# Performance work log

Measured on AMD Instinct MI355X. Metric: run time of the kernel, lower is better.

## Reference

```python
import jax, jax.numpy as jnp
import numpy as np

N = 20000      # nodes
E = 320000     # edges (every node has >=1 incoming edge)
IN = 512       # input feature dim
HID = 128      # per-head hidden dim
H = 8          # heads
C = 64         # classes (final layer hidden dim)
SLOPE = 0.01   # torch F.leaky_relu default negative_slope


def _gat_head(x, src, dst, W, b, al, alb, ar, arb):
    # x: [N, D_in]; W: [D_in, D_h]; al/ar: [D_h]; alb/arb: scalar
    ft = x @ W + b                       # [N, D_h]
    a1 = ft @ al + alb                   # [N] dst-side logit
    a2 = ft @ ar + arb                   # [N] src-side logit
    s = jax.nn.leaky_relu(a1[dst] + a2[src], SLOPE)   # [E]
    smax = jax.ops.segment_max(s, dst, num_segments=N)
    e = jnp.exp(s - smax[dst])
    denom = jax.ops.segment_sum(e, dst, num_segments=N)
    w = e / denom[dst]                   # segment softmax over incoming edges
    accum = jax.ops.segment_sum(w[:, None] * ft[src], dst, num_segments=N)
    return jax.nn.elu(accum)             # GATFinalize (no residual)


def setup_inputs() -> dict:
    key = jax.random.key(0)
    ks = jax.random.split(key, 16)

    def lin(k, i, o):
        return (jax.random.normal(k, (i, o), jnp.float32) / np.sqrt(i))

    features = jax.random.normal(ks[0], (N, IN), jnp.float32)
    src = jax.random.randint(ks[1], (E,), 0, N, jnp.int32)
    dst = jnp.concatenate([
        jnp.arange(N, dtype=jnp.int32),
        jax.random.randint(ks[2], (E - N,), 0, N, jnp.int32),
    ])

    # layer 0: H heads, in_dim -> HID
    W0 = jax.random.normal(ks[3], (H, IN, HID), jnp.float32) / np.sqrt(IN)
    b0 = jnp.zeros((H, HID), jnp.float32)
    al0 = jax.random.normal(ks[4], (H, HID), jnp.float32) / np.sqrt(HID)
    alb0 = jnp.zeros((H,), jnp.float32)
    ar0 = jax.random.normal(ks[5], (H, HID), jnp.float32) / np.sqrt(HID)
    arb0 = jnp.zeros((H,), jnp.float32)

    # layer 1: H heads, H*HID -> HID
    W1 = jax.random.normal(ks[6], (H, H * HID, HID), jnp.float32) / np.sqrt(H * HID)
    b1 = jnp.zeros((H, HID), jnp.float32)
    al1 = jax.random.normal(ks[7], (H, HID), jnp.float32) / np.sqrt(HID)
    alb1 = jnp.zeros((H,), jnp.float32)
    ar1 = jax.random.normal(ks[8], (H, HID), jnp.float32) / np.sqrt(HID)
    arb1 = jnp.zeros((H,), jnp.float32)

    # final: single head, H*HID -> C
    Wf = lin(ks[9], H * HID, C)
    bf = jnp.zeros((C,), jnp.float32)
    alf = jax.random.normal(ks[10], (C,), jnp.float32) / np.sqrt(C)
    albf = jnp.zeros((), jnp.float32)
    arf = jax.random.normal(ks[11], (C,), jnp.float32) / np.sqrt(C)
    arbf = jnp.zeros((), jnp.float32)

    return dict(features=features, src=src, dst=dst,
                W0=W0, b0=b0, al0=al0, alb0=alb0, ar0=ar0, arb0=arb0,
                W1=W1, b1=b1, al1=al1, alb1=alb1, ar1=ar1, arb1=arb1,
                Wf=Wf, bf=bf, alf=alf, albf=albf, arf=arf, arbf=arbf)


def reference(features, src, dst,
              W0, b0, al0, alb0, ar0, arb0,
              W1, b1, al1, alb1, ar1, arb1,
              Wf, bf, alf, albf, arf, arbf):
    x = features
    # layer 0: concat heads -> [N, H*HID]
    x = jnp.concatenate([
        _gat_head(x, src, dst, W0[h], b0[h], al0[h], alb0[h], ar0[h], arb0[h])
        for h in range(H)], axis=1)
    # layer 1
    x = jnp.concatenate([
        _gat_head(x, src, dst, W1[h], b1[h], al1[h], alb1[h], ar1[h], arb1[h])
        for h in range(H)], axis=1)
    # final single-head output layer -> [N, C]
    return _gat_head(x, src, dst, Wf, bf, alf, albf, arf, arbf)
```

## Files before the change

kernel.cpp:

```cpp
#include <hip/hip_runtime.h>
#include <math.h>

#define N_NODES 20000
#define N_EDGES 320000
#define D_IN    512
#define D_HID   128
#define N_HEADS 8
#define N_CLS   64

typedef __bf16 bf16x8 __attribute__((ext_vector_type(8)));
typedef float  f32x4  __attribute__((ext_vector_type(4)));

__device__ __forceinline__ float leaky(float x) { return fmaxf(x, 0.01f * x); }

__device__ __forceinline__ unsigned short f2bf(float f) {
    unsigned u = __float_as_uint(f);
    return (unsigned short)((u + 0x7FFFu + ((u >> 16) & 1u)) >> 16);
}
__device__ __forceinline__ float bflo(unsigned v) { return __uint_as_float(v << 16); }
__device__ __forceinline__ float bfhi(unsigned v) { return __uint_as_float(v & 0xffff0000u); }

__device__ __forceinline__ void gl_lds16(const void* g, void* l) {
    __builtin_amdgcn_global_load_lds((const __attribute__((address_space(1))) void*)g,
                                     (__attribute__((address_space(3))) void*)l, 16, 0, 0);
}

__global__ void k_zero(int* __restrict__ p, int n) {
    int i = blockIdx.x * blockDim.x + threadIdx.x;
    if (i < n) p[i] = 0;
}

__global__ void k_count(const int* __restrict__ dst, int* __restrict__ counts, int e) {
    int i = blockIdx.x * blockDim.x + threadIdx.x;
    if (i < e) atomicAdd(&counts[dst[i]], 1);
}

__global__ void k_scan(const int* __restrict__ counts, int* __restrict__ indptr,
                       int* __restrict__ cursor, int n) {
    __shared__ int sdata[1024];
    __shared__ int srun;
    int t = threadIdx.x;
    if (t == 0) srun = 0;
    __syncthreads();
    for (int base = 0; base < n; base += 1024) {
        int idx = base + t;
        int v = (idx < n) ? counts[idx] : 0;
        sdata[t] = v;
        __syncthreads();
        for (int off = 1; off < 1024; off <<= 1) {
            int x = (t >= off) ? sdata[t - off] : 0;
            __syncthreads();
            sdata[t] += x;
            __syncthreads();
        }
        int incl = sdata[t];
        int run = srun;
        if (idx < n) {
            indptr[idx] = run + incl - v;
            cursor[idx] = run + incl - v;
        }
        __syncthreads();
        if (t == 1023) srun = run + incl;
        __syncthreads();
    }
    if (t == 0) indptr[n] = srun;
}

__global__ void k_scatter(const int* __restrict__ src, const int* __restrict__ dst,
                          int* __restrict__ cursor, int* __restrict__ csr_src, int e) {
    int i = blockIdx.x * blockDim.x + threadIdx.x;
    if (i < e) {
        int pos = atomicAdd(&cursor[dst[i]], 1);
        csr_src[pos] = src[i];
    }
}

__global__ void k_cvtA(const float* __restrict__ in, unsigned short* __restrict__ out, int n4) {
    int i = blockIdx.x * blockDim.x + threadIdx.x;
    if (i < n4) {
        float4 v = ((const float4*)in)[i];
        unsigned long long pk =
            (unsigned long long)f2bf(v.x) | ((unsigned long long)f2bf(v.y) << 16) |
            ((unsigned long long)f2bf(v.z) << 32) | ((unsigned long long)f2bf(v.w) << 48);
        *(unsigned long long*)(out + (size_t)i * 4) = pk;
    }
}

__global__ void k_cvtW(const float* __restrict__ W, unsigned short* __restrict__ Wt,
                       int K, int Nf) {
    __shared__ float t[64][65];
    int k0 = blockIdx.x * 64, n0 = blockIdx.y * 64, h = blockIdx.z;
    const float* Wh = W + (size_t)h * K * Nf;
    unsigned short* Wth = Wt + (size_t)h * K * Nf;
    int tx = threadIdx.x & 63, ty = threadIdx.x >> 6;
#pragma unroll
    for (int i = 0; i < 16; ++i) {
        int k = ty + i * 4;
        t[k][tx] = Wh[(size_t)(k0 + k) * Nf + n0 + tx];
    }
    __syncthreads();
#pragma unroll
    for (int i = 0; i < 16; ++i) {
        int n = ty + i * 4;
        Wth[(size_t)(n0 + n) * K + k0 + tx] = f2bf(t[tx][n]);
    }
}

template<int BN>
__global__ __launch_bounds__(256) void k_gemm_bf16(
    const unsigned short* __restrict__ A, const unsigned short* __restrict__ Bt,
    const float* __restrict__ bias, unsigned short* __restrict__ C,
    int M, int K, int ldc, long strideCh)
{
    constexpr int BM = 128, BK = 64;
    constexpr int WN    = (BN == 128) ? 2 : 1;
    constexpr int MFRAG = (BN == 128) ? 4 : 2;
    constexpr int NFRAG = 4;

    __shared__ unsigned short As[BM * BK];
    __shared__ unsigned short Bs[BN * BK];

    const int tid  = threadIdx.x;
    const int lane = tid & 63;
    const int wid  = tid >> 6;
    const int wm   = wid / WN;
    const int wn   = wid % WN;
    const int m0   = blockIdx.x * BM;
    const int h    = blockIdx.z;

    const unsigned short* Bth = Bt + (size_t)h * BN * K;
    const float* biash = bias + h * BN;
    unsigned short* Ch = C + (size_t)h * strideCh;

    const int rsub = lane & 15;
    const int rhi  = lane >> 4;
    const int wbase = (tid & ~63);

    f32x4 acc[MFRAG][NFRAG];
#pragma unroll
    for (int i = 0; i < MFRAG; ++i)
#pragma unroll
        for (int j = 0; j < NFRAG; ++j) acc[i][j] = (f32x4){0.f, 0.f, 0.f, 0.f};

    for (int k0 = 0; k0 < K; k0 += BK) {
#pragma unroll
        for (int p = 0; p < 4; ++p) {
            int o    = (p * 256 + tid) * 16;
            int row  = o >> 7;
            int icol = (o & 127) ^ ((row & 7) << 4);
            int grow = m0 + row; if (grow > M - 1) grow = M - 1;
            gl_lds16(A + (size_t)grow * K + k0 + (icol >> 1),
                     (void*)((char*)As + (p * 256 + wbase) * 16));
        }
#pragma unroll
        for (int p = 0; p < BN / 32; ++p) {
            int o    = (p * 256 + tid) * 16;
            int row  = o >> 7;
            int icol = (o & 127) ^ ((row & 7) << 4);
            gl_lds16(Bth + (size_t)row * K + k0 + (icol >> 1),
                     (void*)((char*)Bs + (p * 256 + wbase) * 16));
        }
        __syncthreads();

        bf16x8 av[2][MFRAG], bv[2][NFRAG];
#pragma unroll
        for (int q = 0; q < 2; ++q) {
#pragma unroll
            for (int mi = 0; mi < MFRAG; ++mi) {
                int row  = wm * (MFRAG * 16) + mi * 16 + rsub;
                int icol = (q * 64 + rhi * 16) ^ ((row & 7) << 4);
                av[q][mi] = *(const bf16x8*)((const char*)As + row * 128 + icol);
            }
#pragma unroll
            for (int ni = 0; ni < NFRAG; ++ni) {
                int row  = wn * (NFRAG * 16) + ni * 16 + rsub;
                int icol = (q * 64 + rhi * 16) ^ ((row & 7) << 4);
                bv[q][ni] = *(const bf16x8*)((const char*)Bs + row * 128 + icol);
            }
        }
#pragma unroll
        for (int q = 0; q < 2; ++q)
#pragma unroll
            for (int mi = 0; mi < MFRAG; ++mi)
#pragma unroll
                for (int ni = 0; ni < NFRAG; ++ni)
                    acc[mi][ni] = __builtin_amdgcn_mfma_f32_16x16x32_bf16(
                        av[q][mi], bv[q][ni], acc[mi][ni], 0, 0, 0);
        __syncthreads();
    }

#pragma unroll
    for (int ni = 0; ni < NFRAG; ++ni) {
        int col  = wn * (NFRAG * 16) + ni * 16 + rsub;
        float bvv = biash[col];
#pragma unroll
        for (int mi = 0; mi < MFRAG; ++mi) {
            int rowb = m0 + wm * (MFRAG * 16) + mi * 16 + rhi * 4;
#pragma unroll
            for (int r = 0; r < 4; ++r) {
                int row = rowb + r;
                if (row < M) Ch[(size_t)row * ldc + col] = f2bf(acc[mi][ni][r] + bvv);
            }
        }
    }
}

__global__ __launch_bounds__(256) void k_alogit(
    const unsigned short* __restrict__ ft, const float* __restrict__ al,
    const float* __restrict__ alb, const float* __restrict__ ar,
    const float* __restrict__ arb, float* __restrict__ a1,
    float* __restrict__ a2, int H_, int Dh)
{
    int n = blockIdx.x * 4 + (threadIdx.x >> 6);
    int lane = threadIdx.x & 63;
    if (n >= N_NODES) return;
    for (int h = 0; h < H_; ++h) {
        size_t base = ((size_t)h * N_NODES + n) * Dh;
        float s1 = 0.f, s2 = 0.f;
        for (int j0 = 2 * lane; j0 < Dh; j0 += 128) {
            unsigned v = *(const unsigned*)(ft + base + j0);
            float lo = bflo(v), hi = bfhi(v);
            float2 A = *(const float2*)(al + h * Dh + j0);
            float2 R = *(const float2*)(ar + h * Dh + j0);
            s1 += lo * A.x + hi * A.y;
            s2 += lo * R.x + hi * R.y;
        }
#pragma unroll
        for (int off = 32; off > 0; off >>= 1) {
            s1 += __shfl_xor(s1, off);
            s2 += __shfl_xor(s2, off);
        }
        if (lane == 0) {
            a1[n * H_ + h] = s1 + alb[h];
            a2[n * H_ + h] = s2 + arb[h];
        }
    }
}

__global__ __launch_bounds__(256) void k_aggregate8(
    const unsigned short* __restrict__ ft, const float* __restrict__ a1,
    const float* __restrict__ a2, const int* __restrict__ indptr,
    const int* __restrict__ csr_src, unsigned short* __restrict__ outp)
{
    int h = blockIdx.x & 7;
    int n = (blockIdx.x >> 3) * 4 + (threadIdx.x >> 6);
    int lane = threadIdx.x & 63;
    if (n >= N_NODES) return;
    const unsigned short* fth = ft + (size_t)h * N_NODES * 128;
    size_t obase = (size_t)n * 1024 + h * 128;
    int start = indptr[n], end = indptr[n + 1];
    int q   = lane & 15;
    int sub = lane >> 4;

    if (end <= start) {
        if (lane < 16) { uint4 z = make_uint4(0,0,0,0); *(uint4*)(outp + obase + 8 * q) = z; }
        return;
    }
    float a1v = a1[n * 8 + h];

    int sidx0 = 0; float sv0 = 0.f;
    float m = -INFINITY;
    {
        int e = start + lane;
        if (e < end) {
            sidx0 = csr_src[e];
            sv0 = leaky(a1v + a2[sidx0 * 8 + h]);
            m = sv0;
        }
        for (int e2 = start + 64 + lane; e2 < end; e2 += 64)
            m = fmaxf(m, leaky(a1v + a2[csr_src[e2] * 8 + h]));
#pragma unroll
        for (int off = 32; off > 0; off >>= 1) m = fmaxf(m, __shfl_xor(m, off));
    }

    float denom = 0.f;
    float4 accA = make_float4(0.f, 0.f, 0.f, 0.f);
    float4 accB = make_float4(0.f, 0.f, 0.f, 0.f);
    for (int base = start; base < end; base += 64) {
        int ee = base + lane;
        float wgt = 0.f;
        int sidx = sidx0;
        if (base == start) {
            if (ee < end) wgt = expf(sv0 - m);
        } else if (ee < end) {
            sidx = csr_src[ee];
            wgt = expf(leaky(a1v + a2[sidx * 8 + h]) - m);
        }
        denom += wgt;
        int cnt = min(64, end - base);
        for (int i = 0; i < cnt; i += 4) {
            int j  = i + sub;
            int jc = (j < cnt) ? j : i;
            float wj = __shfl(wgt, jc);
            int   sj = __shfl(sidx, jc);
            if (j >= cnt) wj = 0.f;
            uint4 v = *(const uint4*)(fth + (size_t)sj * 128 + 8 * q);
            accA.x += wj * bflo(v.x); accA.y += wj * bfhi(v.x);
            accA.z += wj * bflo(v.y); accA.w += wj * bfhi(v.y);
            accB.x += wj * bflo(v.z); accB.y += wj * bfhi(v.z);
            accB.z += wj * bflo(v.w); accB.w += wj * bfhi(v.w);
        }
    }
#pragma unroll
    for (int off = 32; off > 0; off >>= 1) denom += __shfl_xor(denom, off);
#pragma unroll
    for (int off = 16; off <= 32; off <<= 1) {
        accA.x += __shfl_xor(accA.x, off); accA.y += __shfl_xor(accA.y, off);
        accA.z += __shfl_xor(accA.z, off); accA.w += __shfl_xor(accA.w, off);
        accB.x += __shfl_xor(accB.x, off); accB.y += __shfl_xor(accB.y, off);
        accB.z += __shfl_xor(accB.z, off); accB.w += __shfl_xor(accB.w, off);
    }
    float inv = 1.f / denom;
    if (lane < 16) {
        float r[8] = {accA.x * inv, accA.y * inv, accA.z * inv, accA.w * inv,
                      accB.x * inv, accB.y * inv, accB.z * inv, accB.w * inv};
        unsigned pk[4];
#pragma unroll
        for (int u = 0; u < 4; ++u) {
            float e0 = (r[2*u]   > 0.f) ? r[2*u]   : expm1f(r[2*u]);
            float e1 = (r[2*u+1] > 0.f) ? r[2*u+1] : expm1f(r[2*u+1]);
            pk[u] = (unsigned)f2bf(e0) | ((unsigned)f2bf(e1) << 16);
        }
        *(uint4*)(outp + obase + 8 * q) = make_uint4(pk[0], pk[1], pk[2], pk[3]);
    }
}

__global__ __launch_bounds__(256) void k_aggregate_final(
    const unsigned short* __restrict__ ft, const float* __restrict__ a1,
    const float* __restrict__ a2, const int* __restrict__ indptr,
    const int* __restrict__ csr_src, float* __restrict__ outp)
{
    int n = blockIdx.x * 4 + (threadIdx.x >> 6);
    int lane = threadIdx.x & 63;
    if (n >= N_NODES) return;
    size_t obase = (size_t)n * 64;
    int start = indptr[n], end = indptr[n + 1];

    if (end <= start) {
        if (lane < 32) *(float2*)(outp + obase + 2 * lane) = make_float2(0.f, 0.f);
        return;
    }
    float a1v = a1[n];

    int sidx0 = 0; float sv0 = 0.f;
    float m = -INFINITY;
    {
        int e = start + lane;
        if (e < end) {
            sidx0 = csr_src[e];
            sv0 = leaky(a1v + a2[sidx0]);
            m = sv0;
        }
        for (int e2 = start + 64 + lane; e2 < end; e2 += 64)
            m = fmaxf(m, leaky(a1v + a2[csr_src[e2]]));
#pragma unroll
        for (int off = 32; off > 0; off >>= 1) m = fmaxf(m, __shfl_xor(m, off));
    }

    float denom = 0.f, acc0 = 0.f, acc1 = 0.f;
    for (int base = start; base < end; base += 64) {
        int e = base + lane;
        float wgt = 0.f;
        int sidx = sidx0;
        if (base == start) {
            if (e < end) wgt = expf(sv0 - m);
        } else if (e < end) {
            sidx = csr_src[e];
            wgt = expf(leaky(a1v + a2[sidx]) - m);
        }
        denom += wgt;
        int cnt = min(64, end - base);
        int half = lane >> 5, idx = lane & 31;
        for (int i = 0; i < cnt; i += 2) {
            int j = i + half;
            float wj = (j < cnt) ? __shfl(wgt, j) : 0.f;
            int   sj = __shfl(sidx, (j < cnt) ? j : i);
            unsigned v = *(const unsigned*)(ft + (size_t)sj * 64 + 2 * idx);
            acc0 += wj * bflo(v);
            acc1 += wj * bfhi(v);
        }
    }
#pragma unroll
    for (int off = 32; off > 0; off >>= 1) denom += __shfl_xor(denom, off);
    float inv = 1.f / denom;

    acc0 += __shfl_xor(acc0, 32);
    acc1 += __shfl_xor(acc1, 32);
    float r0 = acc0 * inv, r1 = acc1 * inv;
    r0 = (r0 > 0.f) ? r0 : expm1f(r0);
    r1 = (r1 > 0.f) ? r1 : expm1f(r1);
    if (lane < 32)
        *(float2*)(outp + obase + 2 * lane) = make_float2(r0, r1);
}

extern "C" void kernel_launch(void* const* d_in, const int* in_sizes, int n_in,
                              void* d_out, int out_size, void* d_ws, size_t ws_size,
                              hipStream_t stream) {
    const float* features = (const float*)d_in[0];
    const int*   src      = (const int*)d_in[1];
    const int*   dst      = (const int*)d_in[2];
    const float* W0  = (const float*)d_in[3];
    const float* b0  = (const float*)d_in[4];
    const float* al0 = (const float*)d_in[5];
    const float* alb0= (const float*)d_in[6];
    const float* ar0 = (const float*)d_in[7];
    const float* arb0= (const float*)d_in[8];
    const float* W1  = (const float*)d_in[9];
    const float* b1  = (const float*)d_in[10];
    const float* al1 = (const float*)d_in[11];
    const float* alb1= (const float*)d_in[12];
    const float* ar1 = (const float*)d_in[13];
    const float* arb1= (const float*)d_in[14];
    const float* Wf  = (const float*)d_in[15];
    const float* bff = (const float*)d_in[16];
    const float* alf = (const float*)d_in[17];
    const float* albf= (const float*)d_in[18];
    const float* arf = (const float*)d_in[19];
    const float* arbf= (const float*)d_in[20];
    float* out = (float*)d_out;

    char* wp = (char*)d_ws;
    unsigned short* ft16  = (unsigned short*)wp;  wp += (size_t)N_NODES * 1024 * 2;
    unsigned short* xb16  = (unsigned short*)wp;  wp += (size_t)N_NODES * 1024 * 2;
    unsigned short* feat16= (unsigned short*)wp;  wp += (size_t)N_NODES * 512 * 2;
    unsigned short* w0t   = (unsigned short*)wp;  wp += (size_t)N_HEADS * D_HID * D_IN * 2;
    unsigned short* w1t   = (unsigned short*)wp;  wp += (size_t)N_HEADS * D_HID * 1024 * 2;
    unsigned short* wft   = (unsigned short*)wp;  wp += (size_t)N_CLS * 1024 * 2;
    float* a1             = (float*)wp;           wp += (size_t)N_NODES * N_HEADS * 4;
    float* a2             = (float*)wp;           wp += (size_t)N_NODES * N_HEADS * 4;
    int* counts = (int*)wp;                       wp += (size_t)N_NODES * 4;
    int* indptr = (int*)wp;                       wp += (size_t)(N_NODES + 1) * 4;
    int* cursor = (int*)wp;                       wp += (size_t)N_NODES * 4;
    int* csr    = (int*)wp;

    k_zero<<<(N_NODES + 255) / 256, 256, 0, stream>>>(counts, N_NODES);
    k_count<<<(N_EDGES + 255) / 256, 256, 0, stream>>>(dst, counts, N_EDGES);
    k_scan<<<1, 1024, 0, stream>>>(counts, indptr, cursor, N_NODES);
    k_scatter<<<(N_EDGES + 255) / 256, 256, 0, stream>>>(src, dst, cursor, csr, N_EDGES);

    k_cvtA<<<(N_NODES * D_IN / 4 + 255) / 256, 256, 0, stream>>>(features, feat16, N_NODES * D_IN / 4);
    k_cvtW<<<dim3(D_IN / 64, D_HID / 64, N_HEADS), 256, 0, stream>>>(W0, w0t, D_IN, D_HID);
    k_cvtW<<<dim3(1024 / 64, D_HID / 64, N_HEADS), 256, 0, stream>>>(W1, w1t, 1024, D_HID);
    k_cvtW<<<dim3(1024 / 64, N_CLS / 64, 1), 256, 0, stream>>>(Wf, wft, 1024, N_CLS);

    const int gm = (N_NODES + 127) / 128;
    int nodeBlocks = (N_NODES + 3) / 4;
    int aggBlocksH = 8 * nodeBlocks;

    const long slab = (long)N_NODES * D_HID;

    k_gemm_bf16<128><<<dim3(gm, 1, N_HEADS), 256, 0, stream>>>(
        feat16, w0t, b0, ft16, N_NODES, D_IN, D_HID, slab);
    k_alogit<<<nodeBlocks, 256, 0, stream>>>(ft16, al0, alb0, ar0, arb0, a1, a2, N_HEADS, D_HID);
    k_aggregate8<<<aggBlocksH, 256, 0, stream>>>(ft16, a1, a2, indptr, csr, xb16);

    k_gemm_bf16<128><<<dim3(gm, 1, N_HEADS), 256, 0, stream>>>(
        xb16, w1t, b1, ft16, N_NODES, 1024, D_HID, slab);
    k_alogit<<<nodeBlocks, 256, 0, stream>>>(ft16, al1, alb1, ar1, arb1, a1, a2, N_HEADS, D_HID);
    k_aggregate8<<<aggBlocksH, 256, 0, stream>>>(ft16, a1, a2, indptr, csr, xb16);

    k_gemm_bf16<64><<<dim3(gm, 1, 1), 256, 0, stream>>>(
        xb16, wft, bff, ft16, N_NODES, 1024, N_CLS, 0);
    k_alogit<<<nodeBlocks, 256, 0, stream>>>(ft16, alf, albf, arf, arbf, a1, a2, 1, N_CLS);
    k_aggregate_final<<<nodeBlocks, 256, 0, stream>>>(ft16, a1, a2, indptr, csr, out);
}
```

Measured before the change: 660.7 us.

## Fuse attention logits into GEMM epilogue and batch loads in aggregation loops

Replaces the per-head GEMM plus separate logit kernel with a fused GEMM that computes two heads per block (256-wide N tile) and reduces the al/ar dot products from the fp32 accumulators in the epilogue. This removes the k_alogit pass and its reread of ft for the two hidden layers. The aggregation kernels are also unrolled to issue several independent gathers before accumulating, which raises memory-level parallelism. The cost is higher register pressure from the 4x8 accumulator array, which may lower occupancy, and logits now come from fp32 values rather than the rounded bf16 features.

```diff
diff --git a/kernel.cpp b/kernel.cpp
--- a/kernel.cpp
+++ b/kernel.cpp
@@ -106,41 +106,36 @@
     }
 }
 
-template<int BN>
-__global__ __launch_bounds__(256) void k_gemm_bf16(
+__global__ __launch_bounds__(256) void k_gemm_fused(
     const unsigned short* __restrict__ A, const unsigned short* __restrict__ Bt,
-    const float* __restrict__ bias, unsigned short* __restrict__ C,
-    int M, int K, int ldc, long strideCh)
+    const float* __restrict__ bias, const float* __restrict__ al,
+    const float* __restrict__ alb, const float* __restrict__ ar,
+    const float* __restrict__ arb, unsigned short* __restrict__ C,
+    float* __restrict__ a1, float* __restrict__ a2, int M, int K)
 {
-    constexpr int BM = 128, BK = 64;
-    constexpr int WN    = (BN == 128) ? 2 : 1;
-    constexpr int MFRAG = (BN == 128) ? 4 : 2;
-    constexpr int NFRAG = 4;
-
+    constexpr int BM = 128, BK = 64, BNP = 256;
     __shared__ unsigned short As[BM * BK];
-    __shared__ unsigned short Bs[BN * BK];
+    __shared__ unsigned short Bs[BNP * BK];
 
     const int tid  = threadIdx.x;
     const int lane = tid & 63;
     const int wid  = tid >> 6;
-    const int wm   = wid / WN;
-    const int wn   = wid % WN;
+    const int wm   = wid >> 1;
+    const int wn   = wid & 1;
     const int m0   = blockIdx.x * BM;
-    const int h    = blockIdx.z;
-
-    const unsigned short* Bth = Bt + (size_t)h * BN * K;
-    const float* biash = bias + h * BN;
-    unsigned short* Ch = C + (size_t)h * strideCh;
-
+    const int h0   = blockIdx.z * 2;
+    const int h    = h0 + wn;
+
+    const unsigned short* Bth = Bt + (size_t)h0 * 128 * K;
     const int rsub = lane & 15;
     const int rhi  = lane >> 4;
-    const int wbase = (tid & ~63);
-
-    f32x4 acc[MFRAG][NFRAG];
-#pragma unroll
-    for (int i = 0; i < MFRAG; ++i)
-#pragma unroll
-        for (int j = 0; j < NFRAG; ++j) acc[i][j] = (f32x4){0.f, 0.f, 0.f, 0.f};
+    const int wbase = tid & ~63;
+
+    f32x4 acc[4][8];
+#pragma unroll
+    for (int i = 0; i < 4; ++i)
+#pragma unroll
+        for (int j = 0; j < 8; ++j) acc[i][j] = (f32x4){0.f, 0.f, 0.f, 0.f};
 
     for (int k0 = 0; k0 < K; k0 += BK) {
 #pragma unroll
@@ -153,7 +148,7 @@
                      (void*)((char*)As + (p * 256 + wbase) * 16));
         }
 #pragma unroll
-        for (int p = 0; p < BN / 32; ++p) {
+        for (int p = 0; p < 8; ++p) {
             int o    = (p * 256 + tid) * 16;
             int row  = o >> 7;
             int icol = (o & 127) ^ ((row & 7) << 4);
@@ -162,6 +157,139 @@
         }
         __syncthreads();
 
+#pragma unroll
+        for (int q = 0; q < 2; ++q) {
+            bf16x8 av[4], bv[8];
+#pragma unroll
+            for (int mi = 0; mi < 4; ++mi) {
+                int row  = wm * 64 + mi * 16 + rsub;
+                int icol = (q * 64 + rhi * 16) ^ ((row & 7) << 4);
+                av[mi] = *(const bf16x8*)((const char*)As + row * 128 + icol);
+            }
+#pragma unroll
+            for (int ni = 0; ni < 8; ++ni) {
+                int row  = wn * 128 + ni * 16 + rsub;
+                int icol = (q * 64 + rhi * 16) ^ ((row & 7) << 4);
+                bv[ni] = *(const bf16x8*)((const char*)Bs + row * 128 + icol);
+            }
+#pragma unroll
+            for (int mi = 0; mi < 4; ++mi)
+#pragma unroll
+                for (int ni = 0; ni < 8; ++ni)
+                    acc[mi][ni] = __builtin_amdgcn_mfma_f32_16x16x32_bf16(
+                        av[mi], bv[ni], acc[mi][ni], 0, 0, 0);
+        }
+        __syncthreads();
+    }
+
+#pragma unroll
+    for (int ni = 0; ni < 8; ++ni) {
+        float bvv = bias[h * 128 + ni * 16 + rsub];
+#pragma unroll
+        for (int mi = 0; mi < 4; ++mi)
+#pragma unroll
+            for (int r = 0; r < 4; ++r) acc[mi][ni][r] += bvv;
+    }
+
+    unsigned short* Ch = C + (size_t)h * N_NODES * 128;
+#pragma unroll
+    for (int ni = 0; ni < 8; ++ni) {
+        int col = ni * 16 + rsub;
+#pragma unroll
+        for (int mi = 0; mi < 4; ++mi) {
+            int rowb = m0 + wm * 64 + mi * 16 + rhi * 4;
+#pragma unroll
+            for (int r = 0; r < 4; ++r) {
+                int row = rowb + r;
+                if (row < M) Ch[(size_t)row * 128 + col] = f2bf(acc[mi][ni][r]);
+            }
+        }
+    }
+
+    float alv[8], arv[8];
+#pragma unroll
+    for (int ni = 0; ni < 8; ++ni) {
+        alv[ni] = al[h * 128 + ni * 16 + rsub];
+        arv[ni] = ar[h * 128 + ni * 16 + rsub];
+    }
+    float albv = alb[h], arbv = arb[h];
+#pragma unroll
+    for (int mi = 0; mi < 4; ++mi) {
+#pragma unroll
+        for (int r = 0; r < 4; ++r) {
+            float s1 = 0.f, s2 = 0.f;
+#pragma unroll
+            for (int ni = 0; ni < 8; ++ni) {
+                s1 += acc[mi][ni][r] * alv[ni];
+                s2 += acc[mi][ni][r] * arv[ni];
+            }
+#pragma unroll
+            for (int off = 1; off <= 8; off <<= 1) {
+                s1 += __shfl_xor(s1, off);
+                s2 += __shfl_xor(s2, off);
+            }
+            if (rsub == 0) {
+                int row = m0 + wm * 64 + mi * 16 + rhi * 4 + r;
+                if (row < M) {
+                    a1[row * 8 + h] = s1 + albv;
+                    a2[row * 8 + h] = s2 + arbv;
+                }
+            }
+        }
+    }
+}
+
+template<int BN>
+__global__ __launch_bounds__(256) void k_gemm_bf16(
+    const unsigned short* __restrict__ A, const unsigned short* __restrict__ Bt,
+    const float* __restrict__ bias, unsigned short* __restrict__ C,
+    int M, int K, int ldc)
+{
+    constexpr int BM = 128, BK = 64;
+    constexpr int WN    = 1;
+    constexpr int MFRAG = 2;
+    constexpr int NFRAG = 4;
+
+    __shared__ unsigned short As[BM * BK];
+    __shared__ unsigned short Bs[BN * BK];
+
+    const int tid  = threadIdx.x;
+    const int lane = tid & 63;
+    const int wid  = tid >> 6;
+    const int wm   = wid / WN;
+    const int wn   = wid % WN;
+    const int m0   = blockIdx.x * BM;
+
+    const int rsub = lane & 15;
+    const int rhi  = lane >> 4;
+    const int wbase = tid & ~63;
+
+    f32x4 acc[MFRAG][NFRAG];
+#pragma unroll
+    for (int i = 0; i < MFRAG; ++i)
+#pragma unroll
+        for (int j = 0; j < NFRAG; ++j) acc[i][j] = (f32x4){0.f, 0.f, 0.f, 0.f};
+
+    for (int k0 = 0; k0 < K; k0 += BK) {
+#pragma unroll
+        for (int p = 0; p < 4; ++p) {
+            int o    = (p * 256 + tid) * 16;
+            int row  = o >> 7;
+            int icol = (o & 127) ^ ((row & 7) << 4);
+            int grow = m0 + row; if (grow > M - 1) grow = M - 1;
+            gl_lds16(A + (size_t)grow * K + k0 + (icol >> 1),
+                     (void*)((char*)As + (p * 256 + wbase) * 16));
+        }
+#pragma unroll
+        for (int p = 0; p < BN / 32; ++p) {
+            int o    = (p * 256 + tid) * 16;
+            int row  = o >> 7;
+            int icol = (o & 127) ^ ((row & 7) << 4);
+            gl_lds16(Bt + (size_t)row * K + k0 + (icol >> 1),
+                     (void*)((char*)Bs + (p * 256 + wbase) * 16));
+        }
+        __syncthreads();
+
         bf16x8 av[2][MFRAG], bv[2][NFRAG];
 #pragma unroll
         for (int q = 0; q < 2; ++q) {
@@ -192,14 +320,14 @@
 #pragma unroll
     for (int ni = 0; ni < NFRAG; ++ni) {
         int col  = wn * (NFRAG * 16) + ni * 16 + rsub;
-        float bvv = biash[col];
+        float bvv = bias[col];
 #pragma unroll
         for (int mi = 0; mi < MFRAG; ++mi) {
             int rowb = m0 + wm * (MFRAG * 16) + mi * 16 + rhi * 4;
 #pragma unroll
             for (int r = 0; r < 4; ++r) {
                 int row = rowb + r;
-                if (row < M) Ch[(size_t)row * ldc + col] = f2bf(acc[mi][ni][r] + bvv);
+                if (row < M) C[(size_t)row * ldc + col] = f2bf(acc[mi][ni][r] + bvv);
             }
         }
     }
@@ -253,7 +381,7 @@
     int sub = lane >> 4;
 
     if (end <= start) {
-        if (lane < 16) { uint4 z = make_uint4(0,0,0,0); *(uint4*)(outp + obase + 8 * q) = z; }
+        if (lane < 16) { uint4 z = make_uint4(0, 0, 0, 0); *(uint4*)(outp + obase + 8 * q) = z; }
         return;
     }
     float a1v = a1[n * 8 + h];
@@ -288,17 +416,33 @@
         }
         denom += wgt;
         int cnt = min(64, end - base);
-        for (int i = 0; i < cnt; i += 4) {
+
+        auto iss = [&](int i, float& W, int& S, uint4& V) {
             int j  = i + sub;
-            int jc = (j < cnt) ? j : i;
-            float wj = __shfl(wgt, jc);
-            int   sj = __shfl(sidx, jc);
-            if (j >= cnt) wj = 0.f;
-            uint4 v = *(const uint4*)(fth + (size_t)sj * 128 + 8 * q);
-            accA.x += wj * bflo(v.x); accA.y += wj * bfhi(v.x);
-            accA.z += wj * bflo(v.y); accA.w += wj * bfhi(v.y);
-            accB.x += wj * bflo(v.z); accB.y += wj * bfhi(v.z);
-            accB.z += wj * bflo(v.w); accB.w += wj * bfhi(v.w);
+            int jc = (j < cnt) ? j : (cnt - 1);
+            W = __shfl(wgt, jc);
+            S = __shfl(sidx, jc);
+            if (j >= cnt) W = 0.f;
+            V = *(const uint4*)(fth + (size_t)S * 128 + 8 * q);
+        };
+        auto accf = [&](const uint4& V, float W) {
+            accA.x += W * bflo(V.x); accA.y += W * bfhi(V.x);
+            accA.z += W * bflo(V.y); accA.w += W * bfhi(V.y);
+            accB.x += W * bflo(V.z); accB.y += W * bfhi(V.z);
+            accB.z += W * bflo(V.w); accB.w += W * bfhi(V.w);
+        };
+
+        int i = 0;
+        for (; i + 16 <= cnt; i += 16) {
+            float w0, w1, w2, w3; int s0, s1, s2, s3; uint4 v0, v1, v2, v3;
+            iss(i, w0, s0, v0); iss(i + 4, w1, s1, v1);
+            iss(i + 8, w2, s2, v2); iss(i + 12, w3, s3, v3);
+            accf(v0, w0); accf(v1, w1); accf(v2, w2); accf(v3, w3);
+        }
+        for (; i < cnt; i += 8) {
+            float w0, w1; int s0, s1; uint4 v0, v1;
+            iss(i, w0, s0, v0); iss(i + 4, w1, s1, v1);
+            accf(v0, w0); accf(v1, w1);
         }
     }
 #pragma unroll
@@ -358,6 +502,7 @@
     }
 
     float denom = 0.f, acc0 = 0.f, acc1 = 0.f;
+    int half = lane >> 5, idx = lane & 31;
     for (int base = start; base < end; base += 64) {
         int e = base + lane;
         float wgt = 0.f;
@@ -370,14 +515,18 @@
         }
         denom += wgt;
         int cnt = min(64, end - base);
-        int half = lane >> 5, idx = lane & 31;
-        for (int i = 0; i < cnt; i += 2) {
-            int j = i + half;
-            float wj = (j < cnt) ? __shfl(wgt, j) : 0.f;
-            int   sj = __shfl(sidx, (j < cnt) ? j : i);
-            unsigned v = *(const unsigned*)(ft + (size_t)sj * 64 + 2 * idx);
-            acc0 += wj * bflo(v);
-            acc1 += wj * bfhi(v);
+        for (int i = 0; i < cnt; i += 4) {
+            int j0 = i + half, j1 = i + 2 + half;
+            int jc0 = (j0 < cnt) ? j0 : (cnt - 1);
+            int jc1 = (j1 < cnt) ? j1 : (cnt - 1);
+            float w0 = __shfl(wgt, jc0); int s0 = __shfl(sidx, jc0);
+            float w1 = __shfl(wgt, jc1); int s1 = __shfl(sidx, jc1);
+            if (j0 >= cnt) w0 = 0.f;
+            if (j1 >= cnt) w1 = 0.f;
+            unsigned v0 = *(const unsigned*)(ft + (size_t)s0 * 64 + 2 * idx);
+            unsigned v1 = *(const unsigned*)(ft + (size_t)s1 * 64 + 2 * idx);
+            acc0 += w0 * bflo(v0) + w1 * bflo(v1);
+            acc1 += w0 * bfhi(v0) + w1 * bfhi(v1);
         }
     }
 #pragma unroll
@@ -447,20 +596,16 @@
     int nodeBlocks = (N_NODES + 3) / 4;
     int aggBlocksH = 8 * nodeBlocks;
 
-    const long slab = (long)N_NODES * D_HID;
-
-    k_gemm_bf16<128><<<dim3(gm, 1, N_HEADS), 256, 0, stream>>>(
-        feat16, w0t, b0, ft16, N_NODES, D_IN, D_HID, slab);
-    k_alogit<<<nodeBlocks, 256, 0, stream>>>(ft16, al0, alb0, ar0, arb0, a1, a2, N_HEADS, D_HID);
+    k_gemm_fused<<<dim3(gm, 1, N_HEADS / 2), 256, 0, stream>>>(
+        feat16, w0t, b0, al0, alb0, ar0, arb0, ft16, a1, a2, N_NODES, D_IN);
     k_aggregate8<<<aggBlocksH, 256, 0, stream>>>(ft16, a1, a2, indptr, csr, xb16);
 
-    k_gemm_bf16<128><<<dim3(gm, 1, N_HEADS), 256, 0, stream>>>(
-        xb16, w1t, b1, ft16, N_NODES, 1024, D_HID, slab);
-    k_alogit<<<nodeBlocks, 256, 0, stream>>>(ft16, al1, alb1, ar1, arb1, a1, a2, N_HEADS, D_HID);
+    k_gemm_fused<<<dim3(gm, 1, N_HEADS / 2), 256, 0, stream>>>(
+        xb16, w1t, b1, al1, alb1, ar1, arb1, ft16, a1, a2, N_NODES, 1024);
     k_aggregate8<<<aggBlocksH, 256, 0, stream>>>(ft16, a1, a2, indptr, csr, xb16);
 
     k_gemm_bf16<64><<<dim3(gm, 1, 1), 256, 0, stream>>>(
-        xb16, wft, bff, ft16, N_NODES, 1024, N_CLS, 0);
+        xb16, wft, bff, ft16, N_NODES, 1024, N_CLS);
     k_alogit<<<nodeBlocks, 256, 0, stream>>>(ft16, alf, albf, arf, arbf, a1, a2, 1, N_CLS);
     k_aggregate_final<<<nodeBlocks, 256, 0, stream>>>(ft16, a1, a2, indptr, csr, out);
 }
```

Measured after the change: 646.3 us. -2.2%, faster.
